# Performance work log

Measured on AMD Instinct MI355X. Metric: run time of the kernel, lower is better.

The kernel has to match this reference:

```python
import jax, jax.numpy as jnp
import numpy as np

B, NQ, D = 8, 900, 256
NH, NL, NP = 8, 4, 4
DFF = 1024
DH = D // NH
SHAPES = [(100, 100), (50, 50), (25, 25), (13, 13)]
LV = sum(h * w for h, w in SHAPES)


def setup_inputs() -> dict:
    key = jax.random.key(0)
    ks = iter(jax.random.split(key, 40))
    nrm = lambda shape, s=0.02: jax.random.normal(next(ks), shape, jnp.float32) * s
    starts = np.cumsum([0] + [h * w for h, w in SHAPES[:-1]])
    return {
        'query': jax.random.normal(next(ks), (B, NQ, D), jnp.float32),
        'reference_points': jax.random.uniform(next(ks), (B, NQ, NL, 2), jnp.float32),
        'memory': jax.random.normal(next(ks), (B, LV, D), jnp.float32),
        'memory_spatial_shapes': jnp.array(SHAPES, jnp.int32),
        'level_start_index': jnp.array(starts, jnp.int32),
        'memory_key_padding_mask': jnp.zeros((B, LV), bool),
        'in_proj_w': nrm((3 * D, D)), 'in_proj_b': jnp.zeros((3 * D,), jnp.float32),
        'out_proj_w': nrm((D, D)), 'out_proj_b': jnp.zeros((D,), jnp.float32),
        'ln1_g': jnp.ones((D,), jnp.float32), 'ln1_b': jnp.zeros((D,), jnp.float32),
        'value_proj_w': nrm((D, D)), 'value_proj_b': jnp.zeros((D,), jnp.float32),
        'samp_off_w': nrm((NH * NL * NP * 2, D)), 'samp_off_b': nrm((NH * NL * NP * 2,), 1.0),
        'attn_w_w': nrm((NH * NL * NP, D)), 'attn_w_b': jnp.zeros((NH * NL * NP,), jnp.float32),
        'ca_out_w': nrm((D, D)), 'ca_out_b': jnp.zeros((D,), jnp.float32),
        'ln2_g': jnp.ones((D,), jnp.float32), 'ln2_b': jnp.zeros((D,), jnp.float32),
        'ffn_w1': nrm((DFF, D)), 'ffn_b1': jnp.zeros((DFF,), jnp.float32),
        'ffn_w2': nrm((D, DFF)), 'ffn_b2': jnp.zeros((D,), jnp.float32),
        'ln3_g': jnp.ones((D,), jnp.float32), 'ln3_b': jnp.zeros((D,), jnp.float32),
    }


def layer_norm(x, g, b):
    m = x.mean(-1, keepdims=True)
    v = jnp.var(x, axis=-1, keepdims=True)
    return (x - m) * jax.lax.rsqrt(v + 1e-5) * g + b


def self_attention(x, in_w, in_b, out_w, out_b):
    qkv = x @ in_w.T + in_b
    q, k, v = jnp.split(qkv, 3, axis=-1)
    b, n, _ = x.shape
    q = q.reshape(b, n, NH, DH)
    k = k.reshape(b, n, NH, DH)
    v = v.reshape(b, n, NH, DH)
    scores = jnp.einsum('bqhd,bkhd->bhqk', q, k) / jnp.sqrt(jnp.float32(DH))
    attn = jax.nn.softmax(scores, axis=-1)
    o = jnp.einsum('bhqk,bkhd->bqhd', attn, v).reshape(b, n, D)
    return o @ out_w.T + out_b


def ms_deform_attn(value, shapes, loc, aw):
    # value: (B, Lv, NH, DH); loc: (B, Nq, NH, NL, NP, 2) in [0,1]; aw: (B, Nq, NH, NL, NP)
    b, _, nh, dh = value.shape
    nq, p = loc.shape[1], loc.shape[4]
    acc = jnp.zeros((b, nh, nq, dh), value.dtype)
    start = 0
    for lvl, (hl, wl) in enumerate(shapes):
        v = value[:, start:start + hl * wl].transpose(0, 2, 1, 3)  # (B, NH, HW, DH)
        start += hl * wl
        g = loc[:, :, :, lvl]                      # (B, Nq, NH, NP, 2)
        x = g[..., 0] * wl - 0.5
        y = g[..., 1] * hl - 0.5
        x0 = jnp.floor(x); y0 = jnp.floor(y)
        lx = x - x0; ly = y - y0

        def gather(yi, xi):
            valid = (yi >= 0) & (yi < hl) & (xi >= 0) & (xi < wl)
            idx = (jnp.clip(yi, 0, hl - 1) * wl + jnp.clip(xi, 0, wl - 1)).astype(jnp.int32)
            idx = idx.transpose(0, 2, 1, 3).reshape(b, nh, nq * p)
            out = jnp.take_along_axis(v, idx[..., None], axis=2)  # (B, NH, Nq*NP, DH)
            m = valid.transpose(0, 2, 1, 3).reshape(b, nh, nq * p, 1)
            return jnp.where(m, out, 0.0)

        def w_(w):  # (B,Nq,NH,NP) -> (B,NH,Nq*NP,1)
            return w.transpose(0, 2, 1, 3).reshape(b, nh, nq * p, 1)

        samp = (gather(y0, x0) * w_((1 - lx) * (1 - ly))
                + gather(y0, x0 + 1) * w_(lx * (1 - ly))
                + gather(y0 + 1, x0) * w_((1 - lx) * ly)
                + gather(y0 + 1, x0 + 1) * w_(lx * ly))
        samp = samp.reshape(b, nh, nq, p, dh)
        wl_attn = aw[:, :, :, lvl].transpose(0, 2, 1, 3)  # (B, NH, Nq, NP)
        acc = acc + jnp.einsum('bhqpd,bhqp->bhqd', samp, wl_attn)
    return acc.transpose(0, 2, 1, 3).reshape(b, nq, nh * dh)


def reference(query, reference_points, memory, memory_spatial_shapes, level_start_index,
              memory_key_padding_mask, in_proj_w, in_proj_b, out_proj_w, out_proj_b,
              ln1_g, ln1_b, value_proj_w, value_proj_b, samp_off_w, samp_off_b,
              attn_w_w, attn_w_b, ca_out_w, ca_out_b, ln2_g, ln2_b,
              ffn_w1, ffn_b1, ffn_w2, ffn_b2, ln3_g, ln3_b):
    shapes = [(int(h), int(w)) for h, w in np.asarray(memory_spatial_shapes)]
    b, nq, _ = query.shape

    # self-attention + LN residual
    q_sa = self_attention(query, in_proj_w, in_proj_b, out_proj_w, out_proj_b)
    query = layer_norm(query + q_sa, ln1_g, ln1_b)

    # deformable cross-attention
    value = memory @ value_proj_w.T + value_proj_b
    value = jnp.where(memory_key_padding_mask[..., None], 0.0, value)
    value = value.reshape(b, -1, NH, DH)
    offsets = (query @ samp_off_w.T + samp_off_b).reshape(b, nq, NH, NL, NP, 2)
    aw = (query @ attn_w_w.T + attn_w_b).reshape(b, nq, NH, NL * NP)
    aw = jax.nn.softmax(aw, axis=-1).reshape(b, nq, NH, NL, NP)
    normalizer = jnp.stack([memory_spatial_shapes[:, 1], memory_spatial_shapes[:, 0]], -1).astype(query.dtype)  # (NL,2)=(W,H)
    loc = reference_points[:, :, None, :, None, :] + offsets / normalizer[None, None, None, :, None, :]
    q_ca = ms_deform_attn(value, shapes, loc, aw) @ ca_out_w.T + ca_out_b
    query = layer_norm(query + q_ca, ln2_g, ln2_b)

    # FFN + LN residual
    q_ffn = jax.nn.relu(query @ ffn_w1.T + ffn_b1) @ ffn_w2.T + ffn_b2
    return layer_norm(query + q_ffn, ln3_g, ln3_b)
```

## Files before the change

kernel.cpp:

```cpp
#include <hip/hip_runtime.h>
#include <cstddef>

namespace {

constexpr int kB   = 8;
constexpr int kNQ  = 900;
constexpr int kD   = 256;
constexpr int kDFF = 1024;
constexpr int kLV  = 13294;

typedef short bf16x8 __attribute__((ext_vector_type(8)));
typedef float f32x4  __attribute__((ext_vector_type(4)));

__device__ inline unsigned short f2bf(float f) {
  union { float f; unsigned u; } v; v.f = f;
  return (unsigned short)((v.u + 0x7FFF + ((v.u >> 16) & 1)) >> 16);
}

__device__ inline float bf2f(unsigned short u) {
  union { unsigned u; float f; } v; v.u = (unsigned)u << 16;
  return v.f;
}

__device__ inline unsigned cvt_pk_bf16(float a, float b) {
  unsigned r;
  asm("v_cvt_pk_bf16_f32 %0, %1, %2" : "=v"(r) : "v"(a), "v"(b));
  return r;
}

__global__ __launch_bounds__(256) void f32_to_bf16_kernel(
    const float* __restrict__ in, unsigned* __restrict__ out, int n8) {
  int i = blockIdx.x * 256 + threadIdx.x;
  const int stride = gridDim.x * 256;
  for (; i < n8; i += stride) {
    const float4 a = ((const float4*)in)[(size_t)i * 2];
    const float4 b = ((const float4*)in)[(size_t)i * 2 + 1];
    uint4 r;
    r.x = cvt_pk_bf16(a.x, a.y);
    r.y = cvt_pk_bf16(a.z, a.w);
    r.z = cvt_pk_bf16(b.x, b.y);
    r.w = cvt_pk_bf16(b.z, b.w);
    ((uint4*)out)[i] = r;
  }
}

__global__ __launch_bounds__(256, 2) void gemm_val2_kernel(
    const unsigned short* __restrict__ A, const float* __restrict__ W,
    const float* __restrict__ bias, unsigned short* __restrict__ C, int M) {
  __shared__ short Ws[128 * 256];

  const int t  = threadIdx.x;
  const int w  = t >> 6;
  const int l  = t & 63;
  const int lr = l & 15;
  const int lc = l >> 4;
  const int col  = (int)(blockIdx.x >> 8);
  const int slot = (int)(blockIdx.x & 255);
  const int bn = col * 128;
  const int wm = (w >> 1) * 64;
  const int wn = (w & 1) * 64;

#pragma unroll 4
  for (int i = 0; i < 16; ++i) {
    const int idx = i * 256 + t;
    const int row = idx >> 5;
    const int c16 = idx & 31;
    const float* wp = W + (size_t)(bn + row) * 256 + c16 * 8;
    const float4 w0 = *(const float4*)wp;
    const float4 w1 = *(const float4*)(wp + 4);
    uint4 p;
    p.x = cvt_pk_bf16(w0.x, w0.y);
    p.y = cvt_pk_bf16(w0.z, w0.w);
    p.z = cvt_pk_bf16(w1.x, w1.y);
    p.w = cvt_pk_bf16(w1.z, w1.w);
    const int boff = (row * 512 + c16 * 16) ^ ((row & 7) << 4);
    *(uint4*)((char*)Ws + boff) = p;
  }
  __syncthreads();

  float bv[4];
#pragma unroll
  for (int n = 0; n < 4; ++n) bv[n] = bias[bn + wn + n * 16 + lr];

  for (int tile = slot; tile * 128 < M; tile += 256) {
    const int bm = tile * 128;

    const unsigned short* apm[4];
#pragma unroll
    for (int m = 0; m < 4; ++m) {
      int row = bm + wm + m * 16 + lr;
      row = row < M ? row : M - 1;
      apm[m] = A + (size_t)row * 256 + lc * 8;
    }
    bf16x8 af[8][4];
#pragma unroll
    for (int kk = 0; kk < 8; ++kk)
#pragma unroll
      for (int m = 0; m < 4; ++m)
        af[kk][m] = *(const bf16x8*)(apm[m] + kk * 32);

    f32x4 acc[4][4];
#pragma unroll
    for (int m = 0; m < 4; ++m)
#pragma unroll
      for (int n = 0; n < 4; ++n) acc[m][n] = (f32x4){0.f, 0.f, 0.f, 0.f};

#pragma unroll
    for (int kk = 0; kk < 8; ++kk) {
      const int kb = kk * 64 + lc * 16;
      bf16x8 bfr[4];
#pragma unroll
      for (int n = 0; n < 4; ++n) {
        const int row = wn + n * 16 + lr;
        const int boff = (row * 512 + kb) ^ ((row & 7) << 4);
        bfr[n] = *(const bf16x8*)((const char*)Ws + boff);
      }
#pragma unroll
      for (int m = 0; m < 4; ++m)
#pragma unroll
        for (int n = 0; n < 4; ++n)
          acc[m][n] = __builtin_amdgcn_mfma_f32_16x16x32_bf16(af[kk][m], bfr[n], acc[m][n], 0, 0, 0);
    }

#pragma unroll
    for (int m = 0; m < 4; ++m) {
      const int rbase = bm + wm + m * 16 + lc * 4;
#pragma unroll
      for (int n = 0; n < 4; ++n) {
        const int cidx = bn + wn + n * 16 + lr;
#pragma unroll
        for (int j = 0; j < 4; ++j) {
          const int r = rbase + j;
          if (r < M) C[(size_t)r * 256 + cidx] = f2bf(acc[m][n][j] + bv[n]);
        }
      }
    }
  }
}

__global__ __launch_bounds__(256) void gemm_mfma_kernel(
    const float* __restrict__ A, const float* __restrict__ W,
    const float* __restrict__ bias, void* __restrict__ Cv,
    int M, int N, int K, int relu, int out_bf16) {
  __shared__ short As[128 * 64];
  __shared__ short Bs[128 * 64];

  const int t  = threadIdx.x;
  const int bm = blockIdx.y * 128;
  const int bn = blockIdx.x * 128;
  const int w  = t >> 6;
  const int l  = t & 63;
  const int wm = (w >> 1) * 64;
  const int wn = (w & 1) * 64;

  f32x4 acc[4][4];
#pragma unroll
  for (int m = 0; m < 4; ++m)
#pragma unroll
    for (int n = 0; n < 4; ++n) acc[m][n] = (f32x4){0.f, 0.f, 0.f, 0.f};

  float4 pa[8], pw[8];
  auto load_tile = [&](int k0) {
#pragma unroll
    for (int i = 0; i < 8; ++i) {
      const int slot = i * 256 + t;
      const int row  = slot >> 4;
      const int c4   = slot & 15;
      const int ar   = bm + row;
      pa[i] = (ar < M) ? *(const float4*)(A + (size_t)ar * K + k0 + c4 * 4)
                       : make_float4(0.f, 0.f, 0.f, 0.f);
      pw[i] = *(const float4*)(W + (size_t)(bn + row) * K + k0 + c4 * 4);
    }
  };

  load_tile(0);

  for (int k0 = 0;;) {
#pragma unroll
    for (int i = 0; i < 8; ++i) {
      const int slot = i * 256 + t;
      const int row  = slot >> 4;
      const int c4   = slot & 15;
      const int boff = (row * 128 + c4 * 8) ^ ((row & 7) << 4);
      uint2 ap;
      ap.x = cvt_pk_bf16(pa[i].x, pa[i].y);
      ap.y = cvt_pk_bf16(pa[i].z, pa[i].w);
      *(uint2*)((char*)As + boff) = ap;
      uint2 wp;
      wp.x = cvt_pk_bf16(pw[i].x, pw[i].y);
      wp.y = cvt_pk_bf16(pw[i].z, pw[i].w);
      *(uint2*)((char*)Bs + boff) = wp;
    }
    __syncthreads();

    const int knext = k0 + 64;
    if (knext < K) load_tile(knext);

#pragma unroll
    for (int ks = 0; ks < 2; ++ks) {
      const int koff = (ks * 32 + (l >> 4) * 8) * 2;
      bf16x8 af[4], bfr[4];
#pragma unroll
      for (int m = 0; m < 4; ++m) {
        const int row = wm + m * 16 + (l & 15);
        af[m] = *(const bf16x8*)((const char*)As + ((row * 128 + koff) ^ ((row & 7) << 4)));
      }
#pragma unroll
      for (int n = 0; n < 4; ++n) {
        const int row = wn + n * 16 + (l & 15);
        bfr[n] = *(const bf16x8*)((const char*)Bs + ((row * 128 + koff) ^ ((row & 7) << 4)));
      }
#pragma unroll
      for (int m = 0; m < 4; ++m)
#pragma unroll
        for (int n = 0; n < 4; ++n)
          acc[m][n] = __builtin_amdgcn_mfma_f32_16x16x32_bf16(af[m], bfr[n], acc[m][n], 0, 0, 0);
    }

    k0 = knext;
    if (k0 >= K) break;
    __syncthreads();
  }

  const int lr4 = (l >> 4) * 4;
  const int lc  = l & 15;
#pragma unroll
  for (int m = 0; m < 4; ++m) {
    const int rbase = bm + wm + m * 16 + lr4;
#pragma unroll
    for (int n = 0; n < 4; ++n) {
      const int col = bn + wn + n * 16 + lc;
      const float bv = bias[col];
#pragma unroll
      for (int j = 0; j < 4; ++j) {
        const int r = rbase + j;
        if (r < M) {
          float v = acc[m][n][j] + bv;
          if (relu) v = fmaxf(v, 0.f);
          if (out_bf16)
            ((unsigned short*)Cv)[(size_t)r * N + col] = f2bf(v);
          else
            ((float*)Cv)[(size_t)r * N + col] = v;
        }
      }
    }
  }
}

__global__ __launch_bounds__(256) void self_attn_mfma_kernel(
    const unsigned short* __restrict__ qkv, float* __restrict__ out) {
  const int b = blockIdx.y >> 3;
  const int h = blockIdx.y & 7;
  const int t = threadIdx.x;
  const int w = t >> 6;
  const int l = t & 63;
  const int lr = l & 15;
  const int lc = l >> 4;

  __shared__ short Klds[64 * 40];
  __shared__ short Vt[32 * 68];
  __shared__ short Plds[4][2 * 16 * 68];

  const float scale = 0.17677669529663687f;
  const int qb0 = blockIdx.x * 128 + w * 16;

  bf16x8 qf[2] = {};
#pragma unroll
  for (int qt = 0; qt < 2; ++qt) {
    const int qr = qb0 + qt * 64 + lr;
    if (qr < kNQ)
      qf[qt] = *(const bf16x8*)(qkv + ((size_t)(b * kNQ + qr)) * 768 + h * 32 + lc * 8);
  }

  f32x4 o[2][2];
#pragma unroll
  for (int qt = 0; qt < 2; ++qt)
#pragma unroll
    for (int dh = 0; dh < 2; ++dh) o[qt][dh] = (f32x4){0.f, 0.f, 0.f, 0.f};
  const f32x4 zero4 = {0.f, 0.f, 0.f, 0.f};
  float lsum[2] = {0.f, 0.f};

  const int skey = t & 63, sc = t >> 6;
  bf16x8 kreg = {}, vreg = {};
  auto load_kv = [&](int tb) {
    const int kr = tb + skey;
    if (kr < kNQ) {
      const unsigned short* p = qkv + ((size_t)(b * kNQ + kr)) * 768 + h * 32 + sc * 8;
      kreg = *(const bf16x8*)(p + 256);
      vreg = *(const bf16x8*)(p + 512);
    } else {
      kreg = (bf16x8){}; vreg = (bf16x8){};
    }
  };

  load_kv(0);

  for (int tb = 0; tb < kNQ; tb += 64) {
    *(bf16x8*)&Klds[skey * 40 + sc * 8] = kreg;
#pragma unroll
    for (int i = 0; i < 8; ++i) Vt[(sc * 8 + i) * 68 + skey] = vreg[i];
    __syncthreads();

    if (tb + 64 < kNQ) load_kv(tb + 64);

    f32x4 s[2][4];
#pragma unroll
    for (int kt = 0; kt < 4; ++kt) {
      bf16x8 kf = *(const bf16x8*)&Klds[(kt * 16 + lr) * 40 + lc * 8];
      s[0][kt] = __builtin_amdgcn_mfma_f32_16x16x32_bf16(kf, qf[0], zero4, 0, 0, 0);
      s[1][kt] = __builtin_amdgcn_mfma_f32_16x16x32_bf16(kf, qf[1], zero4, 0, 0, 0);
    }

#pragma unroll
    for (int qt = 0; qt < 2; ++qt) {
      short* Pw = Plds[w] + qt * (16 * 68);
      float ls = 0.f;
#pragma unroll
      for (int kt = 0; kt < 4; ++kt) {
        float p[4];
#pragma unroll
        for (int j = 0; j < 4; ++j) {
          const int kg = tb + kt * 16 + lc * 4 + j;
          const float e = __expf(s[qt][kt][j] * scale);
          p[j] = (kg < kNQ) ? e : 0.f;
          ls += p[j];
        }
        uint2 pk;
        pk.x = cvt_pk_bf16(p[0], p[1]);
        pk.y = cvt_pk_bf16(p[2], p[3]);
        *(uint2*)&Pw[lr * 68 + kt * 16 + lc * 4] = pk;
      }
      lsum[qt] += ls;
    }

    bf16x8 v00 = *(const bf16x8*)&Vt[lr * 68 + lc * 8];
    bf16x8 v01 = *(const bf16x8*)&Vt[lr * 68 + 32 + lc * 8];
    bf16x8 v10 = *(const bf16x8*)&Vt[(16 + lr) * 68 + lc * 8];
    bf16x8 v11 = *(const bf16x8*)&Vt[(16 + lr) * 68 + 32 + lc * 8];
#pragma unroll
    for (int qt = 0; qt < 2; ++qt) {
      const short* Pw = Plds[w] + qt * (16 * 68);
      bf16x8 pa0 = *(const bf16x8*)&Pw[lr * 68 + lc * 8];
      bf16x8 pa1 = *(const bf16x8*)&Pw[lr * 68 + 32 + lc * 8];
      o[qt][0] = __builtin_amdgcn_mfma_f32_16x16x32_bf16(pa0, v00, o[qt][0], 0, 0, 0);
      o[qt][0] = __builtin_amdgcn_mfma_f32_16x16x32_bf16(pa1, v01, o[qt][0], 0, 0, 0);
      o[qt][1] = __builtin_amdgcn_mfma_f32_16x16x32_bf16(pa0, v10, o[qt][1], 0, 0, 0);
      o[qt][1] = __builtin_amdgcn_mfma_f32_16x16x32_bf16(pa1, v11, o[qt][1], 0, 0, 0);
    }
    __syncthreads();
  }

#pragma unroll
  for (int qt = 0; qt < 2; ++qt) {
    float lt = lsum[qt];
    lt += __shfl_xor(lt, 16);
    lt += __shfl_xor(lt, 32);
#pragma unroll
    for (int j = 0; j < 4; ++j) {
      const float lq = __shfl(lt, lc * 4 + j);
      const int q = qb0 + qt * 64 + lc * 4 + j;
      if (q < kNQ) {
        const float inv = 1.f / lq;
        float* op = out + ((size_t)(b * kNQ + q)) * 256 + h * 32;
        op[lr]      = o[qt][0][j] * inv;
        op[16 + lr] = o[qt][1][j] * inv;
      }
    }
  }
}

__global__ __launch_bounds__(256) void ln_res_kernel(
    const float* __restrict__ x, const float* __restrict__ res,
    const float* __restrict__ g, const float* __restrict__ bta,
    float* __restrict__ out) {
  const int row = blockIdx.x;
  const int t = threadIdx.x;
  const size_t idx = (size_t)row * 256 + t;
  const float v = x[idx] + res[idx];
  float s = v, s2 = v * v;
#pragma unroll
  for (int mask = 1; mask < 64; mask <<= 1) {
    s  += __shfl_xor(s, mask);
    s2 += __shfl_xor(s2, mask);
  }
  __shared__ float ws[4], ws2[4];
  if ((t & 63) == 0) { ws[t >> 6] = s; ws2[t >> 6] = s2; }
  __syncthreads();
  const float S  = ws[0] + ws[1] + ws[2] + ws[3];
  const float S2 = ws2[0] + ws2[1] + ws2[2] + ws2[3];
  const float mean = S * (1.f / 256.f);
  const float var  = S2 * (1.f / 256.f) - mean * mean;
  const float rstd = rsqrtf(var + 1e-5f);
  out[idx] = (v - mean) * rstd * g[t] + bta[t];
}

__global__ __launch_bounds__(256) void deform_kernel(
    const unsigned short* __restrict__ value,
    const float* __restrict__ offs,
    const float* __restrict__ awr,
    const float* __restrict__ refp,
    float* __restrict__ out) {
  const int bq = blockIdx.x;
  const int b = bq / kNQ;
  const int t = threadIdx.x;

  __shared__ int2  cpk[128][4];
  __shared__ float part[4][256];

  if (t < 128) {
    const float a = awr[(size_t)bq * 128 + t];
    float mx = a;
#pragma unroll
    for (int mask = 1; mask < 16; mask <<= 1) mx = fmaxf(mx, __shfl_xor(mx, mask));
    const float e = __expf(a - mx);
    float se = e;
#pragma unroll
    for (int mask = 1; mask < 16; mask <<= 1) se += __shfl_xor(se, mask);
    const float aw = e / se;

    const int h = t >> 4, lp = t & 15, lvl = lp >> 2;
    const int HL[4] = {100, 50, 25, 13};
    const int WL[4] = {100, 50, 25, 13};
    const int ST[4] = {0, 10000, 12500, 13125};
    const int Hl = HL[lvl], Wl = WL[lvl], st = ST[lvl];
    const float rx = refp[((size_t)bq * 4 + lvl) * 2 + 0];
    const float ry = refp[((size_t)bq * 4 + lvl) * 2 + 1];
    const float ox = offs[(size_t)bq * 256 + h * 32 + lp * 2 + 0];
    const float oy = offs[(size_t)bq * 256 + h * 32 + lp * 2 + 1];
    const float x = rx * (float)Wl + ox - 0.5f;
    const float y = ry * (float)Hl + oy - 0.5f;
    const float x0f = floorf(x), y0f = floorf(y);
    const int x0 = (int)x0f, y0 = (int)y0f;
    const float lx = x - x0f, ly = y - y0f;
    const float wts[4] = {(1.f - lx) * (1.f - ly), lx * (1.f - ly),
                          (1.f - lx) * ly,         lx * ly};
    const int ys[4] = {y0, y0, y0 + 1, y0 + 1};
    const int xs[4] = {x0, x0 + 1, x0, x0 + 1};
    const int pos = lp * 8 + h;
#pragma unroll
    for (int c = 0; c < 4; ++c) {
      const int yy = ys[c], xx = xs[c];
      const bool valid = (yy >= 0) && (yy < Hl) && (xx >= 0) && (xx < Wl);
      const int yc = min(max(yy, 0), Hl - 1);
      const int xc = min(max(xx, 0), Wl - 1);
      const float wf = valid ? wts[c] * aw : 0.f;
      cpk[pos][c] = make_int2(st + yc * Wl + xc, __float_as_int(wf));
    }
  }
  __syncthreads();

  const int w  = t >> 6;
  const int q4 = t & 63;
  const int h  = q4 >> 3;
  const int ch = q4 * 4;
  const unsigned short* vb = value + (size_t)b * kLV * 256 + ch;

  float a0 = 0.f, a1 = 0.f, a2 = 0.f, a3 = 0.f;
#pragma unroll
  for (int si = 0; si < 4; ++si) {
    const int s = w * 4 + si;
#pragma unroll
    for (int c = 0; c < 4; ++c) {
      const int2 p = cpk[s * 8 + h][c];
      const float wt = __int_as_float(p.y);
      const uint2 v = *(const uint2*)(vb + (size_t)p.x * 256);
      a0 = fmaf(wt, bf2f((unsigned short)(v.x & 0xffff)), a0);
      a1 = fmaf(wt, bf2f((unsigned short)(v.x >> 16)), a1);
      a2 = fmaf(wt, bf2f((unsigned short)(v.y & 0xffff)), a2);
      a3 = fmaf(wt, bf2f((unsigned short)(v.y >> 16)), a3);
    }
  }
  *(float4*)&part[w][ch] = make_float4(a0, a1, a2, a3);
  __syncthreads();

  out[(size_t)bq * 256 + t] = part[0][t] + part[1][t] + part[2][t] + part[3][t];
}

}

extern "C" void kernel_launch(void* const* d_in, const int* in_sizes, int n_in,
                              void* d_out, int out_size, void* d_ws, size_t ws_size,
                              hipStream_t stream) {
  const float* query  = (const float*)d_in[0];
  const float* refp   = (const float*)d_in[1];
  const float* memory = (const float*)d_in[2];
  const float* in_w  = (const float*)d_in[6];
  const float* in_b  = (const float*)d_in[7];
  const float* out_w = (const float*)d_in[8];
  const float* out_b = (const float*)d_in[9];
  const float* ln1g  = (const float*)d_in[10];
  const float* ln1b  = (const float*)d_in[11];
  const float* vp_w  = (const float*)d_in[12];
  const float* vp_b  = (const float*)d_in[13];
  const float* so_w  = (const float*)d_in[14];
  const float* so_b  = (const float*)d_in[15];
  const float* aw_w  = (const float*)d_in[16];
  const float* aw_b  = (const float*)d_in[17];
  const float* ca_w  = (const float*)d_in[18];
  const float* ca_b  = (const float*)d_in[19];
  const float* ln2g  = (const float*)d_in[20];
  const float* ln2b  = (const float*)d_in[21];
  const float* f1_w  = (const float*)d_in[22];
  const float* f1_b  = (const float*)d_in[23];
  const float* f2_w  = (const float*)d_in[24];
  const float* f2_b  = (const float*)d_in[25];
  const float* ln3g  = (const float*)d_in[26];
  const float* ln3b  = (const float*)d_in[27];
  float* out = (float*)d_out;

  const int MQ = kB * kNQ;
  const int MV = kB * kLV;

  float* ws = (float*)d_ws;
  size_t o = 0;
  float* qkvr = ws;
  float* ffh  = ws;  o += (size_t)MQ * kDFF;
  float* sa   = ws + o;  o += (size_t)MQ * kD;
  float* q1   = ws + o;  o += (size_t)MQ * kD;
  float* valr = ws + o;  o += (size_t)MV * kD;
  float* offs = ws + o;  o += (size_t)MQ * kD;
  float* awr  = ws + o;  o += (size_t)MQ * 128;
  float* dfo  = ws + o;  o += (size_t)MQ * kD;
  float* q2   = ws + o;  o += (size_t)MQ * kD;
  float* tmp  = ws + o;  o += (size_t)MQ * kD;
  (void)ws_size; (void)in_sizes; (void)n_in; (void)out_size;

  unsigned short* qkv_bf = (unsigned short*)qkvr;
  unsigned short* val_bf = (unsigned short*)valr;
  unsigned short* m_bf   = (unsigned short*)(valr + (size_t)MV * kD / 2);

  const dim3 blk(256);
  auto g128 = [](int M, int N) { return dim3((unsigned)((N + 127) / 128), (unsigned)((M + 127) / 128)); };

  f32_to_bf16_kernel<<<2048, blk, 0, stream>>>(memory, (unsigned*)m_bf, MV * kD / 8);
  gemm_mfma_kernel<<<g128(MQ, 768), blk, 0, stream>>>(query, in_w, in_b, qkv_bf, MQ, 768, kD, 0, 1);
  self_attn_mfma_kernel<<<dim3((kNQ + 127) / 128, kB * 8), blk, 0, stream>>>(qkv_bf, sa);
  gemm_mfma_kernel<<<g128(MQ, kD), blk, 0, stream>>>(sa, out_w, out_b, tmp, MQ, kD, kD, 0, 0);
  ln_res_kernel<<<MQ, blk, 0, stream>>>(query, tmp, ln1g, ln1b, q1);
  gemm_val2_kernel<<<512, blk, 0, stream>>>(m_bf, vp_w, vp_b, val_bf, MV);
  gemm_mfma_kernel<<<g128(MQ, kD), blk, 0, stream>>>(q1, so_w, so_b, offs, MQ, kD, kD, 0, 0);
  gemm_mfma_kernel<<<g128(MQ, 128), blk, 0, stream>>>(q1, aw_w, aw_b, awr, MQ, 128, kD, 0, 0);
  deform_kernel<<<MQ, blk, 0, stream>>>(val_bf, offs, awr, refp, dfo);
  gemm_mfma_kernel<<<g128(MQ, kD), blk, 0, stream>>>(dfo, ca_w, ca_b, tmp, MQ, kD, kD, 0, 0);
  ln_res_kernel<<<MQ, blk, 0, stream>>>(q1, tmp, ln2g, ln2b, q2);
  gemm_mfma_kernel<<<g128(MQ, kDFF), blk, 0, stream>>>(q2, f1_w, f1_b, ffh, MQ, kDFF, kD, 1, 0);
  gemm_mfma_kernel<<<g128(MQ, kD), blk, 0, stream>>>(ffh, f2_w, f2_b, tmp, MQ, kD, kDFF, 0, 0);
  ln_res_kernel<<<MQ, blk, 0, stream>>>(q2, tmp, ln3g, ln3b, out);
}
```

Before: 301.1 us.

## Fuse fp32-to-bf16 conversion into value GEMM and merge offset/weight GEMMs

```diff
diff --git a/kernel.cpp b/kernel.cpp
--- a/kernel.cpp
+++ b/kernel.cpp
@@ -28,24 +28,17 @@
   return r;
 }
 
-__global__ __launch_bounds__(256) void f32_to_bf16_kernel(
-    const float* __restrict__ in, unsigned* __restrict__ out, int n8) {
-  int i = blockIdx.x * 256 + threadIdx.x;
-  const int stride = gridDim.x * 256;
-  for (; i < n8; i += stride) {
-    const float4 a = ((const float4*)in)[(size_t)i * 2];
-    const float4 b = ((const float4*)in)[(size_t)i * 2 + 1];
-    uint4 r;
-    r.x = cvt_pk_bf16(a.x, a.y);
-    r.y = cvt_pk_bf16(a.z, a.w);
-    r.z = cvt_pk_bf16(b.x, b.y);
-    r.w = cvt_pk_bf16(b.z, b.w);
-    ((uint4*)out)[i] = r;
-  }
+__device__ inline bf16x8 pack8_hw(float4 a, float4 b) {
+  union { unsigned u[4]; bf16x8 v; } r;
+  r.u[0] = cvt_pk_bf16(a.x, a.y);
+  r.u[1] = cvt_pk_bf16(a.z, a.w);
+  r.u[2] = cvt_pk_bf16(b.x, b.y);
+  r.u[3] = cvt_pk_bf16(b.z, b.w);
+  return r.v;
 }
 
 __global__ __launch_bounds__(256, 2) void gemm_val2_kernel(
-    const unsigned short* __restrict__ A, const float* __restrict__ W,
+    const float* __restrict__ A, const float* __restrict__ W,
     const float* __restrict__ bias, unsigned short* __restrict__ C, int M) {
   __shared__ short Ws[128 * 256];
 
@@ -85,19 +78,13 @@
   for (int tile = slot; tile * 128 < M; tile += 256) {
     const int bm = tile * 128;
 
-    const unsigned short* apm[4];
+    const float* apm[4];
 #pragma unroll
     for (int m = 0; m < 4; ++m) {
       int row = bm + wm + m * 16 + lr;
       row = row < M ? row : M - 1;
       apm[m] = A + (size_t)row * 256 + lc * 8;
     }
-    bf16x8 af[8][4];
-#pragma unroll
-    for (int kk = 0; kk < 8; ++kk)
-#pragma unroll
-      for (int m = 0; m < 4; ++m)
-        af[kk][m] = *(const bf16x8*)(apm[m] + kk * 32);
 
     f32x4 acc[4][4];
 #pragma unroll
@@ -106,20 +93,35 @@
       for (int n = 0; n < 4; ++n) acc[m][n] = (f32x4){0.f, 0.f, 0.f, 0.f};
 
 #pragma unroll
-    for (int kk = 0; kk < 8; ++kk) {
-      const int kb = kk * 64 + lc * 16;
-      bf16x8 bfr[4];
-#pragma unroll
-      for (int n = 0; n < 4; ++n) {
-        const int row = wn + n * 16 + lr;
-        const int boff = (row * 512 + kb) ^ ((row & 7) << 4);
-        bfr[n] = *(const bf16x8*)((const char*)Ws + boff);
-      }
-#pragma unroll
-      for (int m = 0; m < 4; ++m)
-#pragma unroll
-        for (int n = 0; n < 4; ++n)
-          acc[m][n] = __builtin_amdgcn_mfma_f32_16x16x32_bf16(af[kk][m], bfr[n], acc[m][n], 0, 0, 0);
+    for (int kp = 0; kp < 4; ++kp) {
+      float4 a0[2][4], a1[2][4];
+#pragma unroll
+      for (int s = 0; s < 2; ++s)
+#pragma unroll
+        for (int m = 0; m < 4; ++m) {
+          const float* ap = apm[m] + (kp * 2 + s) * 32;
+          a0[s][m] = *(const float4*)ap;
+          a1[s][m] = *(const float4*)(ap + 4);
+        }
+#pragma unroll
+      for (int s = 0; s < 2; ++s) {
+        const int kk = kp * 2 + s;
+        const int kb = kk * 64 + lc * 16;
+        bf16x8 bfr[4];
+#pragma unroll
+        for (int n = 0; n < 4; ++n) {
+          const int row = wn + n * 16 + lr;
+          const int boff = (row * 512 + kb) ^ ((row & 7) << 4);
+          bfr[n] = *(const bf16x8*)((const char*)Ws + boff);
+        }
+#pragma unroll
+        for (int m = 0; m < 4; ++m) {
+          const bf16x8 af = pack8_hw(a0[s][m], a1[s][m]);
+#pragma unroll
+          for (int n = 0; n < 4; ++n)
+            acc[m][n] = __builtin_amdgcn_mfma_f32_16x16x32_bf16(af, bfr[n], acc[m][n], 0, 0, 0);
+        }
+      }
     }
 
 #pragma unroll
@@ -241,6 +243,116 @@
             ((unsigned short*)Cv)[(size_t)r * N + col] = f2bf(v);
           else
             ((float*)Cv)[(size_t)r * N + col] = v;
+        }
+      }
+    }
+  }
+}
+
+__global__ __launch_bounds__(256) void gemm_qoff_kernel(
+    const float* __restrict__ A, const float* __restrict__ soW,
+    const float* __restrict__ soB, const float* __restrict__ awW,
+    const float* __restrict__ awB, float* __restrict__ offs,
+    float* __restrict__ awr, int M) {
+  __shared__ short As[128 * 64];
+  __shared__ short Bs[128 * 64];
+
+  const int t  = threadIdx.x;
+  const int bm = blockIdx.y * 128;
+  const int bn = blockIdx.x * 128;
+  const int w  = t >> 6;
+  const int l  = t & 63;
+  const int wm = (w >> 1) * 64;
+  const int wn = (w & 1) * 64;
+
+  f32x4 acc[4][4];
+#pragma unroll
+  for (int m = 0; m < 4; ++m)
+#pragma unroll
+    for (int n = 0; n < 4; ++n) acc[m][n] = (f32x4){0.f, 0.f, 0.f, 0.f};
+
+  float4 pa[8], pw[8];
+  auto load_tile = [&](int k0) {
+#pragma unroll
+    for (int i = 0; i < 8; ++i) {
+      const int slot = i * 256 + t;
+      const int row  = slot >> 4;
+      const int c4   = slot & 15;
+      const int ar   = bm + row;
+      pa[i] = (ar < M) ? *(const float4*)(A + (size_t)ar * 256 + k0 + c4 * 4)
+                       : make_float4(0.f, 0.f, 0.f, 0.f);
+      const int gn = bn + row;
+      const float* Wp = (gn < 256) ? (soW + (size_t)gn * 256)
+                                   : (awW + (size_t)(gn - 256) * 256);
+      pw[i] = *(const float4*)(Wp + k0 + c4 * 4);
+    }
+  };
+
+  load_tile(0);
+
+  for (int k0 = 0;;) {
+#pragma unroll
+    for (int i = 0; i < 8; ++i) {
+      const int slot = i * 256 + t;
+      const int row  = slot >> 4;
+      const int c4   = slot & 15;
+      const int boff = (row * 128 + c4 * 8) ^ ((row & 7) << 4);
+      uint2 ap;
+      ap.x = cvt_pk_bf16(pa[i].x, pa[i].y);
+      ap.y = cvt_pk_bf16(pa[i].z, pa[i].w);
+      *(uint2*)((char*)As + boff) = ap;
+      uint2 wp;
+      wp.x = cvt_pk_bf16(pw[i].x, pw[i].y);
+      wp.y = cvt_pk_bf16(pw[i].z, pw[i].w);
+      *(uint2*)((char*)Bs + boff) = wp;
+    }
+    __syncthreads();
+
+    const int knext = k0 + 64;
+    if (knext < 256) load_tile(knext);
+
+#pragma unroll
+    for (int ks = 0; ks < 2; ++ks) {
+      const int koff = (ks * 32 + (l >> 4) * 8) * 2;
+      bf16x8 af[4], bfr[4];
+#pragma unroll
+      for (int m = 0; m < 4; ++m) {
+        const int row = wm + m * 16 + (l & 15);
+        af[m] = *(const bf16x8*)((const char*)As + ((row * 128 + koff) ^ ((row & 7) << 4)));
+      }
+#pragma unroll
+      for (int n = 0; n < 4; ++n) {
+        const int row = wn + n * 16 + (l & 15);
+        bfr[n] = *(const bf16x8*)((const char*)Bs + ((row * 128 + koff) ^ ((row & 7) << 4)));
+      }
+#pragma unroll
+      for (int m = 0; m < 4; ++m)
+#pragma unroll
+        for (int n = 0; n < 4; ++n)
+          acc[m][n] = __builtin_amdgcn_mfma_f32_16x16x32_bf16(af[m], bfr[n], acc[m][n], 0, 0, 0);
+    }
+
+    k0 = knext;
+    if (k0 >= 256) break;
+    __syncthreads();
+  }
+
+  const int lr4 = (l >> 4) * 4;
+  const int lc  = l & 15;
+#pragma unroll
+  for (int m = 0; m < 4; ++m) {
+    const int rbase = bm + wm + m * 16 + lr4;
+#pragma unroll
+    for (int n = 0; n < 4; ++n) {
+      const int col = bn + wn + n * 16 + lc;
+      const float bv = (col < 256) ? soB[col] : awB[col - 256];
+#pragma unroll
+      for (int j = 0; j < 4; ++j) {
+        const int r = rbase + j;
+        if (r < M) {
+          const float v = acc[m][n][j] + bv;
+          if (col < 256) offs[(size_t)r * 256 + col] = v;
+          else           awr[(size_t)r * 128 + col - 256] = v;
         }
       }
     }
@@ -527,19 +639,17 @@
 
   unsigned short* qkv_bf = (unsigned short*)qkvr;
   unsigned short* val_bf = (unsigned short*)valr;
-  unsigned short* m_bf   = (unsigned short*)(valr + (size_t)MV * kD / 2);
 
   const dim3 blk(256);
   auto g128 = [](int M, int N) { return dim3((unsigned)((N + 127) / 128), (unsigned)((M + 127) / 128)); };
 
-  f32_to_bf16_kernel<<<2048, blk, 0, stream>>>(memory, (unsigned*)m_bf, MV * kD / 8);
   gemm_mfma_kernel<<<g128(MQ, 768), blk, 0, stream>>>(query, in_w, in_b, qkv_bf, MQ, 768, kD, 0, 1);
   self_attn_mfma_kernel<<<dim3((kNQ + 127) / 128, kB * 8), blk, 0, stream>>>(qkv_bf, sa);
   gemm_mfma_kernel<<<g128(MQ, kD), blk, 0, stream>>>(sa, out_w, out_b, tmp, MQ, kD, kD, 0, 0);
   ln_res_kernel<<<MQ, blk, 0, stream>>>(query, tmp, ln1g, ln1b, q1);
-  gemm_val2_kernel<<<512, blk, 0, stream>>>(m_bf, vp_w, vp_b, val_bf, MV);
-  gemm_mfma_kernel<<<g128(MQ, kD), blk, 0, stream>>>(q1, so_w, so_b, offs, MQ, kD, kD, 0, 0);
-  gemm_mfma_kernel<<<g128(MQ, 128), blk, 0, stream>>>(q1, aw_w, aw_b, awr, MQ, 128, kD, 0, 0);
+  gemm_val2_kernel<<<512, blk, 0, stream>>>(memory, vp_w, vp_b, val_bf, MV);
+  gemm_qoff_kernel<<<dim3(3, (MQ + 127) / 128), blk, 0, stream>>>(
+      q1, so_w, so_b, aw_w, aw_b, offs, awr, MQ);
   deform_kernel<<<MQ, blk, 0, stream>>>(val_bf, offs, awr, refp, dfo);
   gemm_mfma_kernel<<<g128(MQ, kD), blk, 0, stream>>>(dfo, ca_w, ca_b, tmp, MQ, kD, kD, 0, 0);
   ln_res_kernel<<<MQ, blk, 0, stream>>>(q1, tmp, ln2g, ln2b, q2);
```

After: 284.0 us. 5.7% less time.
